# Kernel optimization log

Measured on AMD Instinct MI355X. Metric: run time of the kernel, lower is better.

Reference implementation:

```python
import jax, jax.numpy as jnp
import numpy as np

N_EMBED = 768
N_HEAD = 12

def setup_inputs() -> dict:
    key = jax.random.key(0)
    ks = jax.random.split(key, 5)
    B, T, C = 2, 2048, N_EMBED
    s_in = 1.0 / np.sqrt(C)
    x = jax.random.normal(ks[0], (B, T, C), dtype=jnp.float32)
    W_attn = jax.random.normal(ks[1], (C, 3 * C), dtype=jnp.float32) * s_in
    b_attn = jnp.zeros((3 * C,), dtype=jnp.float32)
    W_proj = jax.random.normal(ks[2], (C, C), dtype=jnp.float32) * s_in
    b_proj = jnp.zeros((C,), dtype=jnp.float32)
    return {"x": x, "W_attn": W_attn, "b_attn": b_attn, "W_proj": W_proj, "b_proj": b_proj}

def reference(x, W_attn, b_attn, W_proj, b_proj):
    B, T, C = x.shape
    H = N_HEAD
    D = C // H
    qkv = x @ W_attn + b_attn                      # [B,T,3C]
    q, k, v = jnp.split(qkv, 3, axis=-1)
    # [B,T,C] -> [B,H,T,D]
    q = q.reshape(B, T, H, D).transpose(0, 2, 1, 3)
    k = k.reshape(B, T, H, D).transpose(0, 2, 1, 3)
    v = v.reshape(B, T, H, D).transpose(0, 2, 1, 3)
    scale = 1.0 / np.sqrt(D).astype(np.float32)
    att = jnp.einsum('bhqd,bhkd->bhqk', q, k) * scale   # [B,H,T,T]
    causal = jnp.tril(jnp.ones((T, T), dtype=bool))
    att = jnp.where(causal, att, -jnp.inf)
    att = jax.nn.softmax(att, axis=-1)
    y = jnp.einsum('bhqk,bhkd->bhqd', att, v)           # [B,H,T,D]
    y = y.transpose(0, 2, 1, 3).reshape(B, T, C)
    return y @ W_proj + b_proj
```

## Files before the change

### kernel.cpp

```cpp
#include <hip/hip_runtime.h>

typedef unsigned short u16;
typedef unsigned int   u32;
typedef __bf16 bf16x8 __attribute__((ext_vector_type(8)));
typedef float  f32x4  __attribute__((ext_vector_type(4)));

#define B_DIM 2
#define T_DIM 2048
#define C_DIM 768
#define H_DIM 12
#define D_DIM 64
#define KD 768

__device__ __forceinline__ u16 f2bf(float f) {
    union { float f; u32 u; } v; v.f = f;
    u32 r = v.u + 0x7FFFu + ((v.u >> 16) & 1u);
    return (u16)(r >> 16);
}

__device__ __forceinline__ u32 cvt_pk_bf16(float lo, float hi) {
    u32 r;
    asm("v_cvt_pk_bf16_f32 %0, %1, %2" : "=v"(r) : "v"(lo), "v"(hi));
    return r;
}

__device__ __forceinline__ float exp2_hw(float x) {
    float r;
    asm("v_exp_f32 %0, %1" : "=v"(r) : "v"(x));
    return r;
}

__device__ __forceinline__ void load_lds16(const void* g, void* l) {
    __builtin_amdgcn_global_load_lds(
        (const __attribute__((address_space(1))) u32*)g,
        (__attribute__((address_space(3))) u32*)l,
        16, 0, 0);
}

__global__ __launch_bounds__(256) void convert_bf16(const float* __restrict__ in,
                                                    u16* __restrict__ out) {
    int i = blockIdx.x * blockDim.x + threadIdx.x;
    float4 v = ((const float4*)in)[i];
    ushort4 o;
    o.x = f2bf(v.x); o.y = f2bf(v.y); o.z = f2bf(v.z); o.w = f2bf(v.w);
    ((ushort4*)out)[i] = o;
}

__global__ __launch_bounds__(256) void transpose_bf16(const float* __restrict__ W,
                                                      u16* __restrict__ Wt,
                                                      int K, int N) {
    __shared__ float tile[32][33];
    int bx = blockIdx.x * 32, by = blockIdx.y * 32;
    int tx = threadIdx.x, ty = threadIdx.y;
#pragma unroll
    for (int i = ty; i < 32; i += 8) tile[i][tx] = W[(size_t)(by + i) * N + bx + tx];
    __syncthreads();
#pragma unroll
    for (int i = ty; i < 32; i += 8) Wt[(size_t)(bx + i) * K + by + tx] = f2bf(tile[tx][i]);
}

template <int EPI, int NJ>
__global__ __launch_bounds__(256)
void gemm_bt(const u16* __restrict__ A, const u16* __restrict__ Bt,
             const float* __restrict__ bias,
             u16* __restrict__ Qb, u16* __restrict__ Kb, u16* __restrict__ Vt,
             float* __restrict__ Cout) {
    __shared__ u16 lA[128 * 64];
    __shared__ u16 lB[NJ * 32 * 64];
    const int tid  = threadIdx.x;
    const int lane = tid & 63, wv = tid >> 6;
    const int lr = lane & 15, lg = lane >> 4;
    const int wm = wv >> 1, wn = wv & 1;
    const int row0 = blockIdx.y * 128, col0 = blockIdx.x * (NJ * 32);

    const f32x4 Z4 = {0.f, 0.f, 0.f, 0.f};
    f32x4 acc[4][NJ];
#pragma unroll
    for (int i = 0; i < 4; i++)
#pragma unroll
        for (int j = 0; j < NJ; j++) acc[i][j] = Z4;

    for (int kt = 0; kt < KD / 64; ++kt) {
#pragma unroll
        for (int i = 0; i < 4; i++) {
            int chunk = wv * 4 + i;
            int row = chunk * 8 + (lane >> 3);
            int el  = (lane & 7) * 8;
            load_lds16(&A[(size_t)(row0 + row) * KD + kt * 64 + el], &lA[chunk * 512]);
        }
#pragma unroll
        for (int i = 0; i < NJ; i++) {
            int chunk = wv * NJ + i;
            int row = chunk * 8 + (lane >> 3);
            int el  = (lane & 7) * 8;
            load_lds16(&Bt[(size_t)(col0 + row) * KD + kt * 64 + el], &lB[chunk * 512]);
        }
        __syncthreads();
#pragma unroll
        for (int kk = 0; kk < 2; kk++) {
            bf16x8 af[4], bfr[NJ];
#pragma unroll
            for (int i = 0; i < 4; i++)
                af[i] = *(const bf16x8*)&lA[(wm * 64 + i * 16 + lr) * 64 + kk * 32 + lg * 8];
#pragma unroll
            for (int j = 0; j < NJ; j++)
                bfr[j] = *(const bf16x8*)&lB[(wn * (NJ * 16) + j * 16 + lr) * 64 + kk * 32 + lg * 8];
#pragma unroll
            for (int i = 0; i < 4; i++)
#pragma unroll
                for (int j = 0; j < NJ; j++)
                    acc[i][j] = __builtin_amdgcn_mfma_f32_16x16x32_bf16(af[i], bfr[j], acc[i][j], 0, 0, 0);
        }
        __syncthreads();
    }

    if (EPI == 0) {
        const int b  = row0 >> 11;
        const int t0 = (row0 & 2047) + wm * 64;
        const float qscale = 0.125f * 1.44269504088896340736f;
#pragma unroll
        for (int i = 0; i < 4; i++) {
#pragma unroll
            for (int j = 0; j < NJ; j++) {
                const int n   = col0 + wn * (NJ * 16) + j * 16 + lr;
                const int seg = n / 768;
                const int nn  = n - seg * 768;
                const int h   = nn >> 6;
                const int d   = nn & 63;
                const float bv = bias[n];
#pragma unroll
                for (int r = 0; r < 4; r++) {
                    const int t = t0 + i * 16 + lg * 4 + r;
                    float v = acc[i][j][r] + bv;
                    if (seg == 0) {
                        Qb[((size_t)(b * H_DIM + h) * T_DIM + t) * D_DIM + d] = f2bf(v * qscale);
                    } else if (seg == 1) {
                        Kb[((size_t)(b * H_DIM + h) * T_DIM + t) * D_DIM + d] = f2bf(v);
                    } else {
                        Vt[((size_t)(b * H_DIM + h) * D_DIM + d) * T_DIM + t] = f2bf(v);
                    }
                }
            }
        }
    } else {
#pragma unroll
        for (int i = 0; i < 4; i++)
#pragma unroll
            for (int j = 0; j < NJ; j++) {
                const int n  = col0 + wn * (NJ * 16) + j * 16 + lr;
                const float bv = bias[n];
#pragma unroll
                for (int r = 0; r < 4; r++) {
                    const int m = row0 + wm * 64 + i * 16 + lg * 4 + r;
                    Cout[(size_t)m * 768 + n] = acc[i][j][r] + bv;
                }
            }
    }
}

union VFrag  { struct { ushort4 lo, hi; } s; bf16x8 v; };
union PFrag  { u32 w[4]; bf16x8 v; };
union QU     { f32x4 f; bf16x8 b; };

#define NPSEG 36

__global__ __launch_bounds__(256)
void attn_kernel(const u16* __restrict__ Qb, const u16* __restrict__ Kb,
                 const u16* __restrict__ Vt, u16* __restrict__ Yb,
                 u16* __restrict__ Yp, float2* __restrict__ Ml) {
    __shared__ u16 ldsK[2][64 * 64];
    __shared__ u16 ldsV[2][64 * 64];

    const int i    = blockIdx.x;
    const int bh   = (i & 7) + 8 * ((i >> 3) % 3);
    const int rank = (i >> 3) / 3;
    int c, s;
    if (rank < 4)       { c = 4 + rank;              s = 0; }
    else if (rank < 12) { c = 8 + ((rank - 4) >> 1); s = (rank - 4) & 1; }
    else if (rank < 24) { c = 12 + (rank - 12) / 3;  s = (rank - 12) % 3; }
    else { int j = rank - 24; c = 4 * (j & 3) + (3 - (j >> 2)); s = c >> 2; }
    const int nseg = (c >> 2) + 1;

    const int b = bh / H_DIM, h = bh % H_DIM;
    const int tid  = threadIdx.x;
    const int lane = tid & 63, wv = tid >> 6;
    const int lr = lane & 15, lg = lane >> 4;
    const int sw = (lr & 7) << 3;
    const int q0 = c * 128;
    const int qbase = q0 + wv * 32;
    const int my_kend = qbase + 32;
    const int k0 = s * 512;
    const int k1 = min(512 * (s + 1), q0 + 128);
    const int nt = (k1 - k0) >> 6;

    const u16* Qp = Qb + (size_t)bh * T_DIM * D_DIM;
    const u16* Kp = Kb + (size_t)bh * T_DIM * D_DIM;
    const u16* Vp = Vt + (size_t)bh * D_DIM * T_DIM;

    QU qf[2][2];
#pragma unroll
    for (int m = 0; m < 2; m++)
#pragma unroll
        for (int dh = 0; dh < 2; dh++)
            qf[m][dh].f = *(const f32x4*)&Qp[(size_t)(qbase + m * 16 + lr) * 64 + dh * 32 + lg * 8];
    asm volatile("" :: "v"(qf[0][0].f), "v"(qf[0][1].f), "v"(qf[1][0].f), "v"(qf[1][1].f));

    const f32x4 Z4 = {0.f, 0.f, 0.f, 0.f};
    f32x4 yacc[2][4];
    float mrun[2] = {-1e30f, -1e30f};
    float lrun[2] = {0.f, 0.f};
#pragma unroll
    for (int m = 0; m < 2; m++)
#pragma unroll
        for (int n = 0; n < 4; n++) yacc[m][n] = Z4;

    const int srow = wv * 16 + (lane >> 3);
    const int scol = (((lane & 7) ^ (lane >> 3)) << 3);

    auto stage = [&](int p, int kc) {
#pragma unroll
        for (int j = 0; j < 2; j++) {
            const int r = srow + j * 8;
            load_lds16(Kp + (size_t)(kc + r) * 64 + scol, &ldsK[p][(wv * 16 + j * 8) * 64]);
            load_lds16(Vp + (size_t)r * T_DIM + kc + scol, &ldsV[p][(wv * 16 + j * 8) * 64]);
        }
    };

    auto compute = [&](int p, int kc) {
        QU k0f[4], k1f[4];
#pragma unroll
        for (int kf = 0; kf < 4; kf++) {
            const u16* krow = &ldsK[p][(kf * 16 + lr) * 64];
            k0f[kf].f = *(const f32x4*)&krow[(lg * 8) ^ sw];
            k1f[kf].f = *(const f32x4*)&krow[(32 + lg * 8) ^ sw];
        }
        f32x4 S[2][4];
#pragma unroll
        for (int m = 0; m < 2; m++)
#pragma unroll
            for (int kf = 0; kf < 4; kf++) S[m][kf] = Z4;
        __builtin_amdgcn_s_setprio(1);
#pragma unroll
        for (int kf = 0; kf < 4; kf++)
#pragma unroll
            for (int m = 0; m < 2; m++) {
                S[m][kf] = __builtin_amdgcn_mfma_f32_16x16x32_bf16(k0f[kf].b, qf[m][0].b, S[m][kf], 0, 0, 0);
                S[m][kf] = __builtin_amdgcn_mfma_f32_16x16x32_bf16(k1f[kf].b, qf[m][1].b, S[m][kf], 0, 0, 0);
            }
        __builtin_amdgcn_s_setprio(0);

        if (kc + 63 > qbase) {
#pragma unroll
            for (int m = 0; m < 2; m++) {
                const int q = qbase + m * 16 + lr;
#pragma unroll
                for (int kf = 0; kf < 4; kf++)
#pragma unroll
                    for (int r = 0; r < 4; r++) {
                        const int k = kc + kf * 16 + 4 * lg + r;
                        if (k > q) S[m][kf][r] = -1e30f;
                    }
            }
        }

        PFrag pf[2][2];
#pragma unroll
        for (int m = 0; m < 2; m++) {
            float mx = -1e30f;
#pragma unroll
            for (int kf = 0; kf < 4; kf++) {
                float a = fmaxf(S[m][kf][0], S[m][kf][1]);
                float cm = fmaxf(S[m][kf][2], S[m][kf][3]);
                mx = fmaxf(mx, fmaxf(a, cm));
            }
            mx = fmaxf(mx, __shfl_xor(mx, 16));
            mx = fmaxf(mx, __shfl_xor(mx, 32));
            if (!__all(mx <= mrun[m] + 8.0f)) {
                float mnew = fmaxf(mrun[m], mx);
                float sfr  = exp2_hw(mrun[m] - mnew);
                mrun[m] = mnew;
                lrun[m] *= sfr;
#pragma unroll
                for (int n = 0; n < 4; n++)
#pragma unroll
                    for (int r = 0; r < 4; r++) yacc[m][n][r] *= sfr;
            }
            float sum = 0.f;
#pragma unroll
            for (int kf = 0; kf < 4; kf++)
#pragma unroll
                for (int r = 0; r < 4; r++) {
                    float pb = exp2_hw(S[m][kf][r] - mrun[m]);
                    S[m][kf][r] = pb;
                    sum += pb;
                }
            sum += __shfl_xor(sum, 16);
            sum += __shfl_xor(sum, 32);
            lrun[m] += sum;
#pragma unroll
            for (int sv = 0; sv < 2; sv++) {
                pf[m][sv].w[0] = cvt_pk_bf16(S[m][2 * sv][0],     S[m][2 * sv][1]);
                pf[m][sv].w[1] = cvt_pk_bf16(S[m][2 * sv][2],     S[m][2 * sv][3]);
                pf[m][sv].w[2] = cvt_pk_bf16(S[m][2 * sv + 1][0], S[m][2 * sv + 1][1]);
                pf[m][sv].w[3] = cvt_pk_bf16(S[m][2 * sv + 1][2], S[m][2 * sv + 1][3]);
            }
        }

        __builtin_amdgcn_s_setprio(1);
#pragma unroll
        for (int sv = 0; sv < 2; sv++) {
            VFrag av[4];
#pragma unroll
            for (int n = 0; n < 4; n++) {
                const u16* vrow = &ldsV[p][(n * 16 + lr) * 64];
                av[n].s.lo = *(const ushort4*)&vrow[(sv * 32 + 4 * lg) ^ sw];
                av[n].s.hi = *(const ushort4*)&vrow[(sv * 32 + 16 + 4 * lg) ^ sw];
            }
#pragma unroll
            for (int n = 0; n < 4; n++)
#pragma unroll
                for (int m = 0; m < 2; m++)
                    yacc[m][n] = __builtin_amdgcn_mfma_f32_16x16x32_bf16(av[n].v, pf[m][sv].v, yacc[m][n], 0, 0, 0);
        }
        __builtin_amdgcn_s_setprio(0);
    };

    stage(0, k0);
    for (int t = 0; t < nt; ++t) {
        const int p = t & 1;
        if (t + 1 < nt) {
            stage(p ^ 1, k0 + 64 * (t + 1));
            asm volatile("s_waitcnt vmcnt(4)" ::: "memory");
        } else {
            asm volatile("s_waitcnt vmcnt(0)" ::: "memory");
        }
        __builtin_amdgcn_sched_barrier(0);
        __builtin_amdgcn_s_barrier();
        __builtin_amdgcn_sched_barrier(0);
        if (k0 + 64 * t < my_kend) compute(p, k0 + 64 * t);
        __builtin_amdgcn_sched_barrier(0);
        __builtin_amdgcn_s_barrier();
    }

    if (nseg == 1) {
#pragma unroll
        for (int m = 0; m < 2; m++) {
            const float inv = 1.f / lrun[m];
            const int t2 = qbase + m * 16 + lr;
#pragma unroll
            for (int n = 0; n < 4; n++)
#pragma unroll
                for (int rp = 0; rp < 2; rp++) {
                    u32 dw = cvt_pk_bf16(yacc[m][n][2 * rp] * inv, yacc[m][n][2 * rp + 1] * inv);
                    const int d = n * 16 + 4 * lg + 2 * rp;
                    *(u32*)&Yb[((size_t)(b * T_DIM + t2)) * C_DIM + h * 64 + d] = dw;
                }
        }
    } else {
        const int pidx = (c < 8)  ? (c - 4) * 2 + s
                       : (c < 12) ? 8 + (c - 8) * 3 + s
                                  : 20 + (c - 12) * 4 + s;
        u16* yp = Yp + ((size_t)(bh * NPSEG + pidx)) * 8192;
#pragma unroll
        for (int m = 0; m < 2; m++) {
            const int row = wv * 32 + m * 16 + lr;
#pragma unroll
            for (int n = 0; n < 4; n++)
#pragma unroll
                for (int rp = 0; rp < 2; rp++) {
                    u32 dw = cvt_pk_bf16(yacc[m][n][2 * rp], yacc[m][n][2 * rp + 1]);
                    const int d = n * 16 + 4 * lg + 2 * rp;
                    *(u32*)&yp[row * 64 + d] = dw;
                }
            if (lg == 0) {
                float2 ml; ml.x = mrun[m]; ml.y = lrun[m];
                Ml[((size_t)(bh * NPSEG + pidx)) * 128 + row] = ml;
            }
        }
    }
}

__global__ __launch_bounds__(256)
void attn_merge(const u16* __restrict__ Yp, const float2* __restrict__ Ml,
                u16* __restrict__ Yb) {
    const int bh = blockIdx.x;
    const int c  = 4 + blockIdx.y;
    const int b = bh / H_DIM, h = bh % H_DIM;
    const int nseg  = (c >> 2) + 1;
    const int pbase = (c < 8)  ? (c - 4) * 2
                    : (c < 12) ? 8 + (c - 8) * 3
                               : 20 + (c - 12) * 4;
    const int tid = threadIdx.x;
    const int row = tid >> 1, dh = tid & 1;

    float mv[4], lv[4];
#pragma unroll 4
    for (int s = 0; s < 4; s++) {
        if (s < nseg) {
            float2 t = Ml[((size_t)(bh * NPSEG + pbase + s)) * 128 + row];
            mv[s] = t.x; lv[s] = t.y;
        } else { mv[s] = -1e30f; lv[s] = 0.f; }
    }
    float mstar = fmaxf(fmaxf(mv[0], mv[1]), fmaxf(mv[2], mv[3]));
    float w[4], L = 0.f;
#pragma unroll 4
    for (int s = 0; s < 4; s++) { w[s] = exp2_hw(mv[s] - mstar); L += w[s] * lv[s]; }
    const float inv = 1.f / L;

    const size_t ybase = ((size_t)(bh * NPSEG + pbase)) * 8192 + row * 64 + dh * 32;
    u16* outp = Yb + ((size_t)(b * T_DIM + c * 128 + row)) * C_DIM + h * 64 + dh * 32;
#pragma unroll
    for (int v = 0; v < 4; v++) {
        float acc[8];
#pragma unroll
        for (int j = 0; j < 8; j++) acc[j] = 0.f;
#pragma unroll 4
        for (int s = 0; s < 4; s++) {
            if (s < nseg) {
                bf16x8 yv = *(const bf16x8*)&Yp[ybase + (size_t)s * 8192 + v * 8];
#pragma unroll
                for (int j = 0; j < 8; j++) acc[j] += w[s] * (float)yv[j];
            }
        }
#pragma unroll
        for (int jp = 0; jp < 4; jp++) {
            u32 dw = cvt_pk_bf16(acc[2 * jp] * inv, acc[2 * jp + 1] * inv);
            *(u32*)&outp[v * 8 + jp * 2] = dw;
        }
    }
}

extern "C" void kernel_launch(void* const* d_in, const int* in_sizes, int n_in,
                              void* d_out, int out_size, void* d_ws, size_t ws_size,
                              hipStream_t stream) {
    const float* x      = (const float*)d_in[0];
    const float* W_attn = (const float*)d_in[1];
    const float* b_attn = (const float*)d_in[2];
    const float* W_proj = (const float*)d_in[3];
    const float* b_proj = (const float*)d_in[4];
    float* out = (float*)d_out;

    char* ws = (char*)d_ws;
    u16* xb  = (u16*)(ws);
    u16* WtA = (u16*)(ws + 6291456);
    u16* WtP = (u16*)(ws + 9830400);
    u16* Qb  = (u16*)(ws + 11010048);
    u16* Kb  = (u16*)(ws + 17301504);
    u16* Vt  = (u16*)(ws + 23592960);
    u16* Yb  = (u16*)(ws + 29884416);
    u16* Yp  = (u16*)(ws + 36175872);
    float2* Ml = (float2*)(ws + 50331648);

    convert_bf16<<<3072, 256, 0, stream>>>(x, xb);
    transpose_bf16<<<dim3(2304 / 32, 768 / 32), dim3(32, 8), 0, stream>>>(W_attn, WtA, 768, 2304);
    transpose_bf16<<<dim3(768 / 32, 768 / 32), dim3(32, 8), 0, stream>>>(W_proj, WtP, 768, 768);
    gemm_bt<0, 2><<<dim3(2304 / 64, 4096 / 128), 256, 0, stream>>>(xb, WtA, b_attn, Qb, Kb, Vt, nullptr);
    attn_kernel<<<960, 256, 0, stream>>>(Qb, Kb, Vt, Yb, Yp, Ml);
    attn_merge<<<dim3(B_DIM * H_DIM, 12), 256, 0, stream>>>(Yp, Ml, Yb);
    gemm_bt<1, 2><<<dim3(768 / 64, 4096 / 128), 256, 0, stream>>>(Yb, WtP, b_proj, nullptr, nullptr, nullptr, out);
}
```

Before: 113.2 us.

## Double-buffer GEMM LDS tiles with XOR swizzle and MFMA priority boost

The bf16 GEMM kernel now keeps two LDS buffers per operand. It issues the global-to-LDS loads for the next k-tile before computing on the current one, and uses an explicit vmcnt wait plus barriers in place of the old load-sync-compute-sync sequence. LDS columns are XOR-swizzled by row to cut bank conflicts on the fragment reads, and s_setprio raises wave priority around the MFMA block. This doubles LDS use, which may lower occupancy. The hardcoded vmcnt(6) assumes each stage issues at least six loads, which holds only for some NJ values.

```diff
diff --git a/kernel.cpp b/kernel.cpp
--- a/kernel.cpp
+++ b/kernel.cpp
@@ -65,12 +65,14 @@
              const float* __restrict__ bias,
              u16* __restrict__ Qb, u16* __restrict__ Kb, u16* __restrict__ Vt,
              float* __restrict__ Cout) {
-    __shared__ u16 lA[128 * 64];
-    __shared__ u16 lB[NJ * 32 * 64];
+    __shared__ u16 lA[2][128 * 64];
+    __shared__ u16 lB[2][NJ * 32 * 64];
     const int tid  = threadIdx.x;
     const int lane = tid & 63, wv = tid >> 6;
     const int lr = lane & 15, lg = lane >> 4;
     const int wm = wv >> 1, wn = wv & 1;
+    const int sw = (lr & 7) << 3;
+    const int scol = (((lane & 7) ^ (lane >> 3)) << 3);
     const int row0 = blockIdx.y * 128, col0 = blockIdx.x * (NJ * 32);
 
     const f32x4 Z4 = {0.f, 0.f, 0.f, 0.f};
@@ -80,38 +82,56 @@
 #pragma unroll
         for (int j = 0; j < NJ; j++) acc[i][j] = Z4;
 
-    for (int kt = 0; kt < KD / 64; ++kt) {
+    auto stage = [&](int p, int kt) {
 #pragma unroll
         for (int i = 0; i < 4; i++) {
             int chunk = wv * 4 + i;
             int row = chunk * 8 + (lane >> 3);
-            int el  = (lane & 7) * 8;
-            load_lds16(&A[(size_t)(row0 + row) * KD + kt * 64 + el], &lA[chunk * 512]);
+            load_lds16(&A[(size_t)(row0 + row) * KD + kt * 64 + scol], &lA[p][chunk * 512]);
         }
 #pragma unroll
         for (int i = 0; i < NJ; i++) {
             int chunk = wv * NJ + i;
             int row = chunk * 8 + (lane >> 3);
-            int el  = (lane & 7) * 8;
-            load_lds16(&Bt[(size_t)(col0 + row) * KD + kt * 64 + el], &lB[chunk * 512]);
-        }
-        __syncthreads();
+            load_lds16(&Bt[(size_t)(col0 + row) * KD + kt * 64 + scol], &lB[p][chunk * 512]);
+        }
+    };
+
+    auto compute = [&](int p) {
 #pragma unroll
         for (int kk = 0; kk < 2; kk++) {
             bf16x8 af[4], bfr[NJ];
 #pragma unroll
             for (int i = 0; i < 4; i++)
-                af[i] = *(const bf16x8*)&lA[(wm * 64 + i * 16 + lr) * 64 + kk * 32 + lg * 8];
+                af[i] = *(const bf16x8*)&lA[p][(wm * 64 + i * 16 + lr) * 64 + ((kk * 32 + lg * 8) ^ sw)];
 #pragma unroll
             for (int j = 0; j < NJ; j++)
-                bfr[j] = *(const bf16x8*)&lB[(wn * (NJ * 16) + j * 16 + lr) * 64 + kk * 32 + lg * 8];
+                bfr[j] = *(const bf16x8*)&lB[p][(wn * (NJ * 16) + j * 16 + lr) * 64 + ((kk * 32 + lg * 8) ^ sw)];
+            __builtin_amdgcn_s_setprio(1);
 #pragma unroll
             for (int i = 0; i < 4; i++)
 #pragma unroll
                 for (int j = 0; j < NJ; j++)
                     acc[i][j] = __builtin_amdgcn_mfma_f32_16x16x32_bf16(af[i], bfr[j], acc[i][j], 0, 0, 0);
-        }
-        __syncthreads();
+            __builtin_amdgcn_s_setprio(0);
+        }
+    };
+
+    stage(0, 0);
+    for (int kt = 0; kt < KD / 64; ++kt) {
+        const int p = kt & 1;
+        if (kt + 1 < KD / 64) {
+            stage(p ^ 1, kt + 1);
+            asm volatile("s_waitcnt vmcnt(6)" ::: "memory");
+        } else {
+            asm volatile("s_waitcnt vmcnt(0)" ::: "memory");
+        }
+        __builtin_amdgcn_sched_barrier(0);
+        __builtin_amdgcn_s_barrier();
+        __builtin_amdgcn_sched_barrier(0);
+        compute(p);
+        __builtin_amdgcn_sched_barrier(0);
+        __builtin_amdgcn_s_barrier();
     }
 
     if (EPI == 0) {
```

After: 106.1 us (median of 2 runs). -6.3%, faster.
